# Optimization experiments

Measured on AMD Instinct MI355X. Metric: run time of the kernel, lower is better.

## Reference

```python
import jax, jax.numpy as jnp
import numpy as np

SPAN = 2  # matches init_kwargs

def setup_inputs() -> dict:
    key = jax.random.key(0)
    x = jax.random.normal(key, (16, 512, 512, 32), dtype=jnp.float32)
    return {"x": x}

def reference(x):
    # Original: zero-pad H,W by span, build 3*span+1 rolled copies, concat on
    # channel axis, max over that axis (which also maxes over channels), crop.
    # max(concat(copies), axis=-1) == max over copies of max over channels,
    # so reduce channels first, then take a running max over the shifts —
    # identical math without the (3*span+1)x concat blowup.
    span = SPAN
    xp = jnp.pad(x, ((0, 0), (span, span), (span, span), (0, 0)))
    xc = jnp.max(xp, axis=-1)  # [B, H+2s, W+2s]
    y = xc
    for i in range(1, span + 1):
        # tf.roll(x, i, axis): rolled[h] = x[h-i]; wrap only pulls in zero pad
        # for the cropped interior, matching the original exactly.
        r1 = jnp.roll(xc, i, axis=1)
        r2 = jnp.roll(xc, i, axis=2)
        r12 = jnp.roll(r1, i, axis=2)
        y = jnp.maximum(jnp.maximum(y, r1), jnp.maximum(r2, r12))
    # crop padding border, add trailing singleton channel dim -> [B,H,W,1]
    return y[:, span:-span, span:-span][..., None]
```

## Files before the change

### kernel.cpp

```cpp
#include <hip/hip_runtime.h>


#define HH 512
#define WW 512
#define CC 32
#define TILE 64
#define REG (TILE + 2)
#define LSTR REG

__global__ __launch_bounds__(256) void maxassign2d_kernel(
    const float* __restrict__ x, float* __restrict__ out) {
  __shared__ float m[REG * LSTR];

  const int b  = blockIdx.z;
  const int h0 = blockIdx.y * TILE;
  const int w0 = blockIdx.x * TILE;
  const int tid = threadIdx.x;

  for (int p = tid; p < REG * REG; p += 256) {
    const int rr = p / REG;
    const int cc = p - rr * REG;
    const int h = h0 + rr - 2;
    const int w = w0 + cc - 2;
    float v = 0.0f;
    if (h >= 0 && w >= 0) {
      const float4* px =
          (const float4*)(x + (((size_t)b * HH + h) * WW + w) * CC);
      float4 a0 = px[0], a1 = px[1], a2 = px[2], a3 = px[3];
      float4 a4 = px[4], a5 = px[5], a6 = px[6], a7 = px[7];
      float m0 = fmaxf(fmaxf(a0.x, a0.y), fmaxf(a0.z, a0.w));
      float m1 = fmaxf(fmaxf(a1.x, a1.y), fmaxf(a1.z, a1.w));
      float m2 = fmaxf(fmaxf(a2.x, a2.y), fmaxf(a2.z, a2.w));
      float m3 = fmaxf(fmaxf(a3.x, a3.y), fmaxf(a3.z, a3.w));
      float m4 = fmaxf(fmaxf(a4.x, a4.y), fmaxf(a4.z, a4.w));
      float m5 = fmaxf(fmaxf(a5.x, a5.y), fmaxf(a5.z, a5.w));
      float m6 = fmaxf(fmaxf(a6.x, a6.y), fmaxf(a6.z, a6.w));
      float m7 = fmaxf(fmaxf(a7.x, a7.y), fmaxf(a7.z, a7.w));
      v = fmaxf(fmaxf(fmaxf(m0, m1), fmaxf(m2, m3)),
                fmaxf(fmaxf(m4, m5), fmaxf(m6, m7)));
    }
    m[rr * LSTR + cc] = v;
  }
  __syncthreads();

  for (int p = tid; p < TILE * TILE; p += 256) {
    const int r = p >> 6;
    const int c = p & (TILE - 1);
    const float* base = &m[r * LSTR + c];
    float v = base[2 * LSTR + 2];
    v = fmaxf(v, base[2 * LSTR + 1]);
    v = fmaxf(v, base[1 * LSTR + 2]);
    v = fmaxf(v, base[1 * LSTR + 1]);
    v = fmaxf(v, base[2 * LSTR + 0]);
    v = fmaxf(v, base[0 * LSTR + 2]);
    v = fmaxf(v, base[0 * LSTR + 0]);
    out[((size_t)b * HH + (h0 + r)) * WW + (w0 + c)] = v;
  }
}

extern "C" void kernel_launch(void* const* d_in, const int* in_sizes, int n_in,
                              void* d_out, int out_size, void* d_ws, size_t ws_size,
                              hipStream_t stream) {
  const float* x = (const float*)d_in[0];
  float* out = (float*)d_out;
  const int B = in_sizes[0] / (HH * WW * CC);
  dim3 grid(WW / TILE, HH / TILE, B);
  maxassign2d_kernel<<<grid, 256, 0, stream>>>(x, out);
}
```

Before: 678.6 us.

## Split pixel loads across 4 lanes with shuffle reduce, smaller tiles, vectorized output

Each pixel's 32 channels are now read by four cooperating lanes, each issuing two float4 loads, and the lane results are combined with xor shuffles. This makes adjacent lanes hit contiguous memory and keeps more loads in flight per wave. Tiles shrink to 32x64 to raise the block count and occupancy (launch bounds 256,8), and the shared-memory stride is padded to 67. The stencil stage now computes four outputs per thread from register-cached rows and writes them with a float4 store. In exchange there is more shuffle and index arithmetic, and halo overhead per tile grows.

```diff
diff --git a/kernel.cpp b/kernel.cpp
--- a/kernel.cpp
+++ b/kernel.cpp
@@ -4,57 +4,88 @@
 #define HH 512
 #define WW 512
 #define CC 32
-#define TILE 64
-#define REG (TILE + 2)
-#define LSTR REG
+#define TH 32
+#define TW 64
+#define RH (TH + 2)
+#define RW (TW + 2)
+#define NPX (RH * RW)
+#define LSTR 67
 
-__global__ __launch_bounds__(256) void maxassign2d_kernel(
+__global__ __launch_bounds__(256, 8) void maxassign2d_kernel(
     const float* __restrict__ x, float* __restrict__ out) {
-  __shared__ float m[REG * LSTR];
+  __shared__ float m[RH * LSTR];
 
-  const int b  = blockIdx.z;
-  const int h0 = blockIdx.y * TILE;
-  const int w0 = blockIdx.x * TILE;
+  const int b   = blockIdx.z;
+  const int h0  = blockIdx.y * TH;
+  const int w0  = blockIdx.x * TW;
   const int tid = threadIdx.x;
 
-  for (int p = tid; p < REG * REG; p += 256) {
-    const int rr = p / REG;
-    const int cc = p - rr * REG;
-    const int h = h0 + rr - 2;
-    const int w = w0 + cc - 2;
-    float v = 0.0f;
-    if (h >= 0 && w >= 0) {
-      const float4* px =
-          (const float4*)(x + (((size_t)b * HH + h) * WW + w) * CC);
-      float4 a0 = px[0], a1 = px[1], a2 = px[2], a3 = px[3];
-      float4 a4 = px[4], a5 = px[5], a6 = px[6], a7 = px[7];
-      float m0 = fmaxf(fmaxf(a0.x, a0.y), fmaxf(a0.z, a0.w));
-      float m1 = fmaxf(fmaxf(a1.x, a1.y), fmaxf(a1.z, a1.w));
-      float m2 = fmaxf(fmaxf(a2.x, a2.y), fmaxf(a2.z, a2.w));
-      float m3 = fmaxf(fmaxf(a3.x, a3.y), fmaxf(a3.z, a3.w));
-      float m4 = fmaxf(fmaxf(a4.x, a4.y), fmaxf(a4.z, a4.w));
-      float m5 = fmaxf(fmaxf(a5.x, a5.y), fmaxf(a5.z, a5.w));
-      float m6 = fmaxf(fmaxf(a6.x, a6.y), fmaxf(a6.z, a6.w));
-      float m7 = fmaxf(fmaxf(a7.x, a7.y), fmaxf(a7.z, a7.w));
-      v = fmaxf(fmaxf(fmaxf(m0, m1), fmaxf(m2, m3)),
-                fmaxf(fmaxf(m4, m5), fmaxf(m6, m7)));
+  const int jj = tid & 3;
+  const int q  = tid >> 2;
+
+  for (unsigned p0 = q; p0 < NPX; p0 += 128) {
+    const unsigned p1 = p0 + 64;
+
+    const unsigned rr0 = p0 / RW;
+    const unsigned cc0 = p0 - rr0 * RW;
+    const int h_0 = h0 + (int)rr0 - 2;
+    const int w_0 = w0 + (int)cc0 - 2;
+    const bool g0 = (h_0 >= 0) && (w_0 >= 0);
+    const float4* px0 =
+        (const float4*)(x + (((long long)b * HH + h_0) * WW + w_0) * CC);
+
+    const unsigned rr1 = p1 / RW;
+    const unsigned cc1 = p1 - rr1 * RW;
+    const int h_1 = h0 + (int)rr1 - 2;
+    const int w_1 = w0 + (int)cc1 - 2;
+    const bool g1 = (p1 < NPX) && (h_1 >= 0) && (w_1 >= 0);
+    const float4* px1 =
+        (const float4*)(x + (((long long)b * HH + h_1) * WW + w_1) * CC);
+
+    const float4 z = make_float4(0.f, 0.f, 0.f, 0.f);
+    float4 a0 = g0 ? px0[jj]     : z;
+    float4 b0 = g0 ? px0[jj + 4] : z;
+    float4 a1 = g1 ? px1[jj]     : z;
+    float4 b1 = g1 ? px1[jj + 4] : z;
+
+    float v0 = fmaxf(fmaxf(fmaxf(a0.x, a0.y), fmaxf(a0.z, a0.w)),
+                     fmaxf(fmaxf(b0.x, b0.y), fmaxf(b0.z, b0.w)));
+    float v1 = fmaxf(fmaxf(fmaxf(a1.x, a1.y), fmaxf(a1.z, a1.w)),
+                     fmaxf(fmaxf(b1.x, b1.y), fmaxf(b1.z, b1.w)));
+
+    v0 = fmaxf(v0, __shfl_xor(v0, 1));
+    v0 = fmaxf(v0, __shfl_xor(v0, 2));
+    v1 = fmaxf(v1, __shfl_xor(v1, 1));
+    v1 = fmaxf(v1, __shfl_xor(v1, 2));
+
+    if (jj == 0) {
+      m[rr0 * LSTR + cc0] = v0;
+      if (p1 < NPX) m[rr1 * LSTR + cc1] = v1;
     }
-    m[rr * LSTR + cc] = v;
   }
   __syncthreads();
 
-  for (int p = tid; p < TILE * TILE; p += 256) {
-    const int r = p >> 6;
-    const int c = p & (TILE - 1);
+  for (int s = tid; s < TH * TW / 4; s += 256) {
+    const int r = s >> 4;
+    const int c = (s & 15) << 2;
     const float* base = &m[r * LSTR + c];
-    float v = base[2 * LSTR + 2];
-    v = fmaxf(v, base[2 * LSTR + 1]);
-    v = fmaxf(v, base[1 * LSTR + 2]);
-    v = fmaxf(v, base[1 * LSTR + 1]);
-    v = fmaxf(v, base[2 * LSTR + 0]);
-    v = fmaxf(v, base[0 * LSTR + 2]);
-    v = fmaxf(v, base[0 * LSTR + 0]);
-    out[((size_t)b * HH + (h0 + r)) * WW + (w0 + c)] = v;
+    float r0[6], r1[6], r2[6];
+#pragma unroll
+    for (int k = 0; k < 6; ++k) {
+      r0[k] = base[k];
+      r1[k] = base[LSTR + k];
+      r2[k] = base[2 * LSTR + k];
+    }
+    float4 v;
+    float* vp = &v.x;
+#pragma unroll
+    for (int k = 0; k < 4; ++k) {
+      const float t0 = fmaxf(r0[k], r0[k + 2]);
+      const float t1 = fmaxf(r1[k + 1], r1[k + 2]);
+      const float t2 = fmaxf(fmaxf(r2[k], r2[k + 1]), r2[k + 2]);
+      vp[k] = fmaxf(fmaxf(t0, t1), t2);
+    }
+    *(float4*)(out + ((long long)b * HH + h0 + r) * WW + w0 + c) = v;
   }
 }
 
@@ -64,6 +95,6 @@
   const float* x = (const float*)d_in[0];
   float* out = (float*)d_out;
   const int B = in_sizes[0] / (HH * WW * CC);
-  dim3 grid(WW / TILE, HH / TILE, B);
+  dim3 grid(WW / TW, HH / TH, B);
   maxassign2d_kernel<<<grid, 256, 0, stream>>>(x, out);
 }
```

Result: slower. 775.0 us (+14.2%).

## Split into coalesced channel-max pass and vectorized shift-max pass via workspace

Applied to the files above, without the earlier changes.

Replaces the fused tiled kernel with two kernels: a grid-stride kernel that reduces channels with fully coalesced float4 loads and warp shuffles into a workspace map, and a second kernel that computes the shifted max with float4 reads and writes. This removes halo recomputation and the per-thread strided 128-byte loads. The cost is an extra write and read of the reduced map through global memory, plus a second launch and a reliance on sufficient workspace.

```diff
diff --git a/kernel.cpp b/kernel.cpp
--- a/kernel.cpp
+++ b/kernel.cpp
@@ -4,58 +4,56 @@
 #define HH 512
 #define WW 512
 #define CC 32
-#define TILE 64
-#define REG (TILE + 2)
-#define LSTR REG
 
-__global__ __launch_bounds__(256) void maxassign2d_kernel(
-    const float* __restrict__ x, float* __restrict__ out) {
-  __shared__ float m[REG * LSTR];
+__global__ __launch_bounds__(256) void chanmax_kernel(
+    const float4* __restrict__ x4, float* __restrict__ M, int nf4) {
+  const int tid = threadIdx.x;
+  const int stride = gridDim.x * 256;
+  for (int f = blockIdx.x * 256 + tid; f < nf4; f += stride) {
+    const float4 v = x4[f];
+    float m = fmaxf(fmaxf(v.x, v.y), fmaxf(v.z, v.w));
+    m = fmaxf(m, __shfl_xor(m, 1));
+    m = fmaxf(m, __shfl_xor(m, 2));
+    m = fmaxf(m, __shfl_xor(m, 4));
+    if ((tid & 7) == 0) M[f >> 3] = m;
+  }
+}
 
-  const int b  = blockIdx.z;
-  const int h0 = blockIdx.y * TILE;
-  const int w0 = blockIdx.x * TILE;
-  const int tid = threadIdx.x;
+__global__ __launch_bounds__(256) void shiftmax_kernel(
+    const float* __restrict__ M, float* __restrict__ out, int total4) {
+  const int g = blockIdx.x * 256 + threadIdx.x;
+  if (g >= total4) return;
+  const int c4 = g & (WW / 4 - 1);
+  const int bh = g >> 7;
+  const int h  = bh & (HH - 1);
 
-  for (int p = tid; p < REG * REG; p += 256) {
-    const int rr = p / REG;
-    const int cc = p - rr * REG;
-    const int h = h0 + rr - 2;
-    const int w = w0 + cc - 2;
-    float v = 0.0f;
-    if (h >= 0 && w >= 0) {
-      const float4* px =
-          (const float4*)(x + (((size_t)b * HH + h) * WW + w) * CC);
-      float4 a0 = px[0], a1 = px[1], a2 = px[2], a3 = px[3];
-      float4 a4 = px[4], a5 = px[5], a6 = px[6], a7 = px[7];
-      float m0 = fmaxf(fmaxf(a0.x, a0.y), fmaxf(a0.z, a0.w));
-      float m1 = fmaxf(fmaxf(a1.x, a1.y), fmaxf(a1.z, a1.w));
-      float m2 = fmaxf(fmaxf(a2.x, a2.y), fmaxf(a2.z, a2.w));
-      float m3 = fmaxf(fmaxf(a3.x, a3.y), fmaxf(a3.z, a3.w));
-      float m4 = fmaxf(fmaxf(a4.x, a4.y), fmaxf(a4.z, a4.w));
-      float m5 = fmaxf(fmaxf(a5.x, a5.y), fmaxf(a5.z, a5.w));
-      float m6 = fmaxf(fmaxf(a6.x, a6.y), fmaxf(a6.z, a6.w));
-      float m7 = fmaxf(fmaxf(a7.x, a7.y), fmaxf(a7.z, a7.w));
-      v = fmaxf(fmaxf(fmaxf(m0, m1), fmaxf(m2, m3)),
-                fmaxf(fmaxf(m4, m5), fmaxf(m6, m7)));
-    }
-    m[rr * LSTR + cc] = v;
+  const float4* row2 = (const float4*)M + (size_t)bh * (WW / 4);
+  const float4* row1 = row2 - WW / 4;
+  const float4* row0 = row2 - 2 * (WW / 4);
+
+  const float4 z = make_float4(0.f, 0.f, 0.f, 0.f);
+  const bool cg = (c4 > 0);
+  const float4 b2 = row2[c4];
+  const float4 a2 = cg ? row2[c4 - 1] : z;
+  const float4 b1 = (h > 0) ? row1[c4] : z;
+  const float4 a1 = (h > 0 && cg) ? row1[c4 - 1] : z;
+  const float4 b0 = (h > 1) ? row0[c4] : z;
+  const float4 a0 = (h > 1 && cg) ? row0[c4 - 1] : z;
+
+  const float c2[6] = {a2.z, a2.w, b2.x, b2.y, b2.z, b2.w};
+  const float c1[6] = {a1.z, a1.w, b1.x, b1.y, b1.z, b1.w};
+  const float c0_[6] = {a0.z, a0.w, b0.x, b0.y, b0.z, b0.w};
+
+  float4 v;
+  float* vp = &v.x;
+#pragma unroll
+  for (int k = 0; k < 4; ++k) {
+    const float t2 = fmaxf(fmaxf(c2[k], c2[k + 1]), c2[k + 2]);
+    const float t1 = fmaxf(c1[k + 1], c1[k + 2]);
+    const float t0 = fmaxf(c0_[k], c0_[k + 2]);
+    vp[k] = fmaxf(fmaxf(t2, t1), t0);
   }
-  __syncthreads();
-
-  for (int p = tid; p < TILE * TILE; p += 256) {
-    const int r = p >> 6;
-    const int c = p & (TILE - 1);
-    const float* base = &m[r * LSTR + c];
-    float v = base[2 * LSTR + 2];
-    v = fmaxf(v, base[2 * LSTR + 1]);
-    v = fmaxf(v, base[1 * LSTR + 2]);
-    v = fmaxf(v, base[1 * LSTR + 1]);
-    v = fmaxf(v, base[2 * LSTR + 0]);
-    v = fmaxf(v, base[0 * LSTR + 2]);
-    v = fmaxf(v, base[0 * LSTR + 0]);
-    out[((size_t)b * HH + (h0 + r)) * WW + (w0 + c)] = v;
-  }
+  ((float4*)out)[g] = v;
 }
 
 extern "C" void kernel_launch(void* const* d_in, const int* in_sizes, int n_in,
@@ -63,7 +61,14 @@
                               hipStream_t stream) {
   const float* x = (const float*)d_in[0];
   float* out = (float*)d_out;
-  const int B = in_sizes[0] / (HH * WW * CC);
-  dim3 grid(WW / TILE, HH / TILE, B);
-  maxassign2d_kernel<<<grid, 256, 0, stream>>>(x, out);
+  float* M = (float*)d_ws;
+
+  const int nfloat = in_sizes[0];
+  const int nf4 = nfloat / 4;
+  const int npix = nfloat / CC;
+  const int total4 = npix / 4;
+
+  chanmax_kernel<<<8192, 256, 0, stream>>>((const float4*)x, M, nf4);
+  const int blocksB = (total4 + 255) / 256;
+  shiftmax_kernel<<<blocksB, 256, 0, stream>>>(M, out, total4);
 }
```

Measured after the change: 684.1 us. No clear change (+0.8%).
